# Kernel tuning notes

Hardware: AMD Instinct MI355X
Metric: run time of the kernel (lower is better)

Reference implementation:

```python
import jax, jax.numpy as jnp
import numpy as np

NEG_SLOPE = 0.01  # torch F.leaky_relu default
BN_EPS = 1e-5
N_GRAPHS = 256


def _bn(x, gamma, beta):
    # training-mode BatchNorm1d per head over the node axis; x: [N, H, O]
    mu = x.mean(axis=0)
    var = x.var(axis=0)
    return (x - mu) * jax.lax.rsqrt(var + BN_EPS) * gamma + beta


def _gat_layer(h, src, dst, snorm, fcW, aS, aD, gamma, beta):
    # h: [N, Din]; fcW: [H, Din, O]; aS/aD/gamma/beta: [H, O]
    N = h.shape[0]
    z = jnp.einsum('nd,hdo->nho', h, fcW)                 # [N, H, O]
    el = jnp.einsum('nho,ho->nh', z, aS)                  # attn_fc src half
    er = jnp.einsum('nho,ho->nh', z, aD)                  # attn_fc dst half
    e = jax.nn.leaky_relu(el[src] + er[dst], NEG_SLOPE)   # [E, H]
    emax = jax.ops.segment_max(e, dst, num_segments=N)    # softmax over in-edges
    ee = jnp.exp(e - emax[dst])
    denom = jax.ops.segment_sum(ee, dst, num_segments=N)
    alpha = ee / denom[dst]                               # [E, H]
    msg = alpha[:, :, None] * z[src]                      # [E, H, O]
    agg = jax.ops.segment_sum(msg, dst, num_segments=N)   # [N, H, O]
    agg = agg * snorm[:, None, None]                      # graph_norm
    agg = _bn(agg, gamma, beta)                           # batch_norm
    out = jax.nn.elu(agg).reshape(N, -1)                  # concat heads
    return h + out                                        # residual (Din == H*O)


def setup_inputs() -> dict:
    key = jax.random.key(0)
    ks = jax.random.split(key, 32)
    N, E, G = 50000, 1600000, N_GRAPHS
    DIN, H, O, D, NC = 128, 8, 16, 128, 10
    L_mid = 3  # L-1 multi-head layers

    graph_ids = jnp.sort(jax.random.randint(ks[0], (N,), 0, G))
    counts = jax.ops.segment_sum(jnp.ones((N,), jnp.float32), graph_ids, num_segments=G)
    snorm = (1.0 / jnp.sqrt(jnp.maximum(counts, 1.0)))[graph_ids]  # nodes_num_norm_sqrt
    src = jax.random.randint(ks[1], (E,), 0, N)
    dst = jax.random.randint(ks[2], (E,), 0, N)

    def nrm(k, shape, s=0.1):
        return jax.random.normal(k, shape, jnp.float32) * s

    return {
        'nodes_feat': jax.random.normal(ks[3], (N, DIN), jnp.float32),
        'snorm': snorm,
        'emb_W': nrm(ks[4], (DIN, D)), 'emb_b': jnp.zeros((D,), jnp.float32),
        'fcW': nrm(ks[5], (L_mid, H, D, O)),
        'aS': nrm(ks[6], (L_mid, H, O)), 'aD': nrm(ks[7], (L_mid, H, O)),
        'gamma': jnp.ones((L_mid, H, O), jnp.float32),
        'beta': jnp.zeros((L_mid, H, O), jnp.float32),
        'fcW_last': nrm(ks[8], (1, D, D)),
        'aS_last': nrm(ks[9], (1, D)), 'aD_last': nrm(ks[10], (1, D)),
        'g_last': jnp.ones((1, D), jnp.float32), 'b_last': jnp.zeros((1, D), jnp.float32),
        'w1': nrm(ks[11], (D, D // 2)), 'b1': jnp.zeros((D // 2,), jnp.float32),
        'w2': nrm(ks[12], (D // 2, D // 4)), 'b2': jnp.zeros((D // 4,), jnp.float32),
        'w3': nrm(ks[13], (D // 4, NC)), 'b3': jnp.zeros((NC,), jnp.float32),
        'src': src, 'dst': dst, 'graph_ids': graph_ids,
    }


def reference(nodes_feat, snorm, emb_W, emb_b, fcW, aS, aD, gamma, beta,
              fcW_last, aS_last, aD_last, g_last, b_last,
              w1, b1, w2, b2, w3, b3, src, dst, graph_ids):
    h = nodes_feat @ emb_W + emb_b                        # embedding_h
    for l in range(fcW.shape[0]):                         # L-1 multi-head GAT layers
        h = _gat_layer(h, src, dst, snorm, fcW[l], aS[l], aD[l], gamma[l], beta[l])
    h = _gat_layer(h, src, dst, snorm, fcW_last, aS_last, aD_last, g_last, b_last)
    # mean_nodes readout over variable-size graphs
    counts = jax.ops.segment_sum(jnp.ones_like(snorm), graph_ids, num_segments=N_GRAPHS)
    hg = jax.ops.segment_sum(h, graph_ids, num_segments=N_GRAPHS)
    hg = hg / jnp.maximum(counts, 1.0)[:, None]           # [G, D]
    # MLPReadout: D -> D/2 -> D/4 -> n_classes
    y = jax.nn.relu(hg @ w1 + b1)
    y = jax.nn.relu(y @ w2 + b2)
    return y @ w3 + b3
```

## Files before the change

kernel.cpp:

```cpp
#include <hip/hip_runtime.h>
#include <hip/hip_bf16.h>
#include <hip/hip_fp16.h>

typedef __hip_bfloat16 bf16;
typedef __attribute__((ext_vector_type(8))) short short8;
typedef __attribute__((ext_vector_type(4))) float floatx4;

__device__ __forceinline__ float ldc(const void* p, size_t i, int code) {
    if (code == 1) return __bfloat162float(((const bf16*)p)[i]);
    if (code == 2) return __half2float(((const __half*)p)[i]);
    return ((const float*)p)[i];
}
__device__ __forceinline__ void stc(void* p, size_t i, int code, float v) {
    if (code == 1) ((bf16*)p)[i] = __float2bfloat16(v);
    else if (code == 2) ((__half*)p)[i] = __float2half(v);
    else ((float*)p)[i] = v;
}
__device__ __forceinline__ unsigned int pk2(float a, float b) {
    unsigned int ua = __float_as_uint(a); ua += 0x7fffu + ((ua >> 16) & 1u);
    unsigned int ub = __float_as_uint(b); ub += 0x7fffu + ((ub >> 16) & 1u);
    return (ua >> 16) | (ub & 0xffff0000u);
}

__global__ void k_detect(const unsigned short* __restrict__ g, int* __restrict__ code) {
    unsigned short a = g[0], b = g[1], c = g[2], d = g[3];
    int r;
    if (a == 0x3F80 && b == 0x3F80 && c == 0x3F80 && d == 0x3F80) r = 1;
    else if (a == 0x3C00 && b == 0x3C00 && c == 0x3C00 && d == 0x3C00) r = 2;
    else r = 3;
    *code = r;
}

__global__ void k_zero_i(int* p, int n) { int i = blockIdx.x * 256 + threadIdx.x; if (i < n) p[i] = 0; }
__global__ void k_zero_f(float* p, int n) { int i = blockIdx.x * 256 + threadIdx.x; if (i < n) p[i] = 0.f; }
__global__ void k_sent(void* o, int n, float v, const int* codep) {
    int code = *codep;
    int i = blockIdx.x * 256 + threadIdx.x;
    if (i < n) stc(o, i, code, v);
}

struct CvtArgs { const void* src[17]; int off[18]; };
__global__ void k_cvt_all(float* __restrict__ dst, CvtArgs a,
                          const int* __restrict__ codep, int total) {
    int i = blockIdx.x * 256 + threadIdx.x;
    if (i >= total) return;
    int code = *codep;
    int seg = 0;
    #pragma unroll
    for (int k = 0; k < 16; ++k) seg += (i >= a.off[k + 1]) ? 1 : 0;
    dst[i] = ldc(a.src[seg], i - a.off[seg], code);
}

#define ETILE 8192
__global__ __launch_bounds__(256) void k_bcount(const int* __restrict__ dst,
        int* __restrict__ bcnt, int E, int nbuck) {
    __shared__ int h[200];
    int t = threadIdx.x;
    for (int i = t; i < nbuck; i += 256) h[i] = 0;
    __syncthreads();
    int e0 = blockIdx.x * ETILE;
    int n = min(ETILE, E - e0);
    for (int i = t; i < n; i += 256) atomicAdd(&h[dst[e0 + i] >> 8], 1);
    __syncthreads();
    for (int i = t; i < nbuck; i += 256)
        if (h[i]) atomicAdd(&bcnt[i], h[i]);
}

__global__ void k_scan(const int* __restrict__ cnt, int* __restrict__ off,
                       int* __restrict__ cur, int n) {
    __shared__ int sums[1024];
    int tid = threadIdx.x;
    int C = (n + 1023) >> 10;
    int lo = tid * C, hi = min(lo + C, n);
    int s = 0;
    for (int i = lo; i < hi; ++i) s += cnt[i];
    sums[tid] = s;
    __syncthreads();
    for (int o = 1; o < 1024; o <<= 1) {
        int v = (tid >= o) ? sums[tid - o] : 0;
        __syncthreads();
        sums[tid] += v;
        __syncthreads();
    }
    int run = (tid > 0) ? sums[tid - 1] : 0;
    for (int i = lo; i < hi; ++i) { off[i] = run; cur[i] = run; run += cnt[i]; }
    if (tid == 1023) off[n] = sums[1023];
}

__global__ __launch_bounds__(256) void k_bscat(const int* __restrict__ src,
        const int* __restrict__ dst, int* __restrict__ bcur,
        unsigned int* __restrict__ ebuf, int E, int nbuck) {
    __shared__ unsigned int eord[ETILE];
    __shared__ int cnt[200], lst[200], cur[200], gb[200];
    int t = threadIdx.x;
    int e0 = blockIdx.x * ETILE;
    int n = min(ETILE, E - e0);
    for (int i = t; i < nbuck; i += 256) cnt[i] = 0;
    __syncthreads();
    for (int i = t; i < n; i += 256) atomicAdd(&cnt[dst[e0 + i] >> 8], 1);
    __syncthreads();
    if (t == 0) {
        int run = 0;
        for (int b = 0; b < nbuck; ++b) { int c = cnt[b]; lst[b] = run; cur[b] = run; run += c; }
    }
    __syncthreads();
    for (int b = t; b < nbuck; b += 256)
        gb[b] = cnt[b] ? atomicAdd(&bcur[b], cnt[b]) : 0;
    for (int i = t; i < n; i += 256) {
        int d = dst[e0 + i];
        int pos = atomicAdd(&cur[d >> 8], 1);
        eord[pos] = ((unsigned int)d << 16) | (unsigned int)src[e0 + i];
    }
    __syncthreads();
    for (int i = t; i < n; i += 256) {
        unsigned int pk = eord[i];
        int b = pk >> 24;
        ebuf[gb[b] + (i - lst[b])] = pk;
    }
}

__global__ __launch_bounds__(256) void k_fscatter(const unsigned int* __restrict__ ebuf,
        const int* __restrict__ boff, int* __restrict__ row_off,
        unsigned short* __restrict__ col_src, int N, int E) {
    __shared__ int cnt[256], cur[256];
    int b = blockIdx.x, t = threadIdx.x;
    int lo = boff[b], hi = boff[b + 1];
    int nodelo = b << 8;
    cnt[t] = 0;
    __syncthreads();
    for (int j = lo + t; j < hi; j += 256)
        atomicAdd(&cnt[(int)(ebuf[j] >> 16) - nodelo], 1);
    __syncthreads();
    if (t == 0) {
        int run = lo;
        for (int i = 0; i < 256; ++i) { int c = cnt[i]; cur[i] = run; cnt[i] = run; run += c; }
    }
    __syncthreads();
    int node = nodelo + t;
    if (node < N) row_off[node] = cnt[t];
    if (t == 0 && b == (int)gridDim.x - 1) row_off[N] = E;
    for (int j = lo + t; j < hi; j += 256) {
        unsigned int pk = ebuf[j];
        int pos = atomicAdd(&cur[(int)(pk >> 16) - nodelo], 1);
        col_src[pos] = (unsigned short)(pk & 0xffffu);
    }
}

#define WB_STRIDE 136
#define WB_MAT 19584
__global__ void k_wtrans(const void* __restrict__ fcW, const void* __restrict__ fcW_last,
                         const void* __restrict__ emb_W,
                         const float* __restrict__ aSf, const float* __restrict__ aDf,
                         const float* __restrict__ aSlf, const float* __restrict__ aDlf,
                         unsigned short* __restrict__ Wb, const int* __restrict__ codep) {
    int code = *codep;
    int idx = blockIdx.x * 256 + threadIdx.x;
    if (idx >= 5 * WB_MAT) return;
    int m = idx / WB_MAT, rem = idx % WB_MAT;
    int c = rem / WB_STRIDE, k = rem % WB_STRIDE;
    float v = 0.f;
    if (k < 128) {
        if (m == 0) {
            if (c < 128) v = ldc(emb_W, k * 128 + c, code);
        } else if (m <= 3) {
            int l = m - 1;
            if (c < 128) v = ldc(fcW, l * 16384 + (c >> 4) * 2048 + k * 16 + (c & 15), code);
            else if (c < 136) {
                int hh = c - 128; float s = 0.f;
                for (int o = 0; o < 16; ++o)
                    s += ldc(fcW, l * 16384 + hh * 2048 + k * 16 + o, code) * aSf[l * 128 + hh * 16 + o];
                v = s;
            } else {
                int hh = c - 136; float s = 0.f;
                for (int o = 0; o < 16; ++o)
                    s += ldc(fcW, l * 16384 + hh * 2048 + k * 16 + o, code) * aDf[l * 128 + hh * 16 + o];
                v = s;
            }
        } else {
            if (c < 128) v = ldc(fcW_last, k * 128 + c, code);
            else if (c == 128) { float s = 0.f; for (int o = 0; o < 128; ++o) s += ldc(fcW_last, k * 128 + o, code) * aSlf[o]; v = s; }
            else if (c == 129) { float s = 0.f; for (int o = 0; o < 128; ++o) s += ldc(fcW_last, k * 128 + o, code) * aDlf[o]; v = s; }
        }
    }
    Wb[idx] = (unsigned short)(pk2(v, 0.f) & 0xffffu);
}

__global__ __launch_bounds__(256) void k_gemm(const void* __restrict__ Av, int a_raw,
        const int* __restrict__ codep, const unsigned short* __restrict__ Wbm,
        const float* __restrict__ bias, float* __restrict__ outf,
        unsigned int* __restrict__ zb,
        float* __restrict__ el, float* __restrict__ er, int H, int N) {
    __shared__ unsigned short Wl[WB_MAT];
    int tid = threadIdx.x;
    {
        const uint4* s4 = (const uint4*)Wbm;
        uint4* d4 = (uint4*)Wl;
        for (int i = tid; i < WB_MAT / 8; i += 256) d4[i] = s4[i];
    }
    int wave = tid >> 6, lane = tid & 63;
    int c15 = lane & 15, quad = lane >> 4;
    int rowb = blockIdx.x * 64 + wave * 16;
    int myrow = rowb + c15;
    bool rowok = myrow < N;
    int code = a_raw ? *codep : 3;

    floatx4 acc[9];
    #pragma unroll
    for (int i = 0; i < 9; ++i) acc[i] = (floatx4){0.f, 0.f, 0.f, 0.f};

    __syncthreads();
    #pragma unroll
    for (int ks = 0; ks < 4; ++ks) {
        int k0 = ks * 32 + quad * 8;
        short8 a;
        if (!rowok) {
            a = (short8){0, 0, 0, 0, 0, 0, 0, 0};
        } else if (code == 1) {
            union { uint4 u; short8 s; } cv;
            cv.u = *(const uint4*)((const unsigned short*)Av + (size_t)myrow * 128 + k0);
            a = cv.s;
        } else if (code == 3) {
            const float* ap = (const float*)Av + (size_t)myrow * 128 + k0;
            float4 x = *(const float4*)ap;
            float4 y = *(const float4*)(ap + 4);
            union { uint4 u; short8 s; } cv;
            cv.u = make_uint4(pk2(x.x, x.y), pk2(x.z, x.w), pk2(y.x, y.y), pk2(y.z, y.w));
            a = cv.s;
        } else {
            const __half* ap = (const __half*)Av + (size_t)myrow * 128 + k0;
            union { uint4 u; short8 s; } cv;
            cv.u = make_uint4(pk2(__half2float(ap[0]), __half2float(ap[1])),
                              pk2(__half2float(ap[2]), __half2float(ap[3])),
                              pk2(__half2float(ap[4]), __half2float(ap[5])),
                              pk2(__half2float(ap[6]), __half2float(ap[7])));
            a = cv.s;
        }
        #pragma unroll
        for (int ct = 0; ct < 9; ++ct) {
            union { uint4 u; short8 s; } bv;
            bv.u = *(const uint4*)&Wl[(ct * 16 + c15) * WB_STRIDE + k0];
            acc[ct] = __builtin_amdgcn_mfma_f32_16x16x32_bf16(a, bv.s, acc[ct], 0, 0, 0);
        }
    }

    if (zb == nullptr) {
        #pragma unroll
        for (int ct = 0; ct < 8; ++ct) {
            int c = ct * 16 + c15;
            float bj = bias ? bias[c] : 0.f;
            #pragma unroll
            for (int r = 0; r < 4; ++r) {
                int n = rowb + quad * 4 + r;
                if (n < N) outf[(size_t)n * 128 + c] = acc[ct][r] + bj;
            }
        }
    } else {
        #pragma unroll
        for (int ct = 0; ct < 8; ++ct) {
            #pragma unroll
            for (int r = 0; r < 4; ++r) {
                float v = acc[ct][r];
                float vx = __shfl_xor(v, 1);
                if ((c15 & 1) == 0) {
                    int n = rowb + quad * 4 + r;
                    if (n < N) zb[(size_t)n * 64 + ct * 8 + (c15 >> 1)] = pk2(v, vx);
                }
            }
        }
        #pragma unroll
        for (int r = 0; r < 4; ++r) {
            int n = rowb + quad * 4 + r;
            if (n < N) {
                float v = acc[8][r];
                if (c15 < H) el[n * H + c15] = v;
                else if (c15 < 2 * H) er[n * H + (c15 - H)] = v;
            }
        }
    }
}

__global__ __launch_bounds__(256) void k_agg(const unsigned int* __restrict__ zb,
        const float* __restrict__ el, const float* __restrict__ er,
        const int* __restrict__ row_off, const unsigned short* __restrict__ col_src,
        const float* __restrict__ snormf, float* __restrict__ agg,
        int N, int H) {
    int n = blockIdx.x * 4 + (threadIdx.x >> 6);
    if (n >= N) return;
    int lane = threadIdx.x & 63;
    int half = lane >> 5;
    int sub = lane & 31;
    int hha = (H == 8) ? (sub >> 2) : 0;
    float er_t = er[n * H + hha];
    float er_w = (H == 8) ? er[n * 8 + (lane >> 3)] : er_t;
    int beg = row_off[n], end = row_off[n + 1];
    float l = 0.f, c0 = 0.f, c1 = 0.f, c2 = 0.f, c3 = 0.f;
    int j = beg;
    if (H == 8) {
        for (; j + 8 <= end; j += 8) {
            int sv = col_src[j + (lane & 7)];
            float e = el[sv * 8 + (lane >> 3)] + er_w;
            e = (e > 0.f) ? e : 0.01f * e;
            float w = __expf(fminf(e, 60.f));
            #pragma unroll
            for (int p = 0; p < 4; ++p) {
                int i = 2 * p + half;
                float wi = __shfl(w, (hha << 3) + i);
                int si = col_src[j + i];
                uint2 v = *(const uint2*)(zb + (size_t)si * 64 + sub * 2);
                l += wi;
                c0 = fmaf(wi, __uint_as_float(v.x << 16), c0);
                c1 = fmaf(wi, __uint_as_float(v.x & 0xffff0000u), c1);
                c2 = fmaf(wi, __uint_as_float(v.y << 16), c2);
                c3 = fmaf(wi, __uint_as_float(v.y & 0xffff0000u), c3);
            }
        }
    } else {
        for (; j + 16 <= end; j += 16) {
            int sv = col_src[j + (lane & 15)];
            float e = el[sv] + er_w;
            e = (e > 0.f) ? e : 0.01f * e;
            float w = __expf(fminf(e, 60.f));
            #pragma unroll
            for (int p = 0; p < 8; ++p) {
                int i = 2 * p + half;
                float wi = __shfl(w, i, 16);
                int si = col_src[j + i];
                uint2 v = *(const uint2*)(zb + (size_t)si * 64 + sub * 2);
                l += wi;
                c0 = fmaf(wi, __uint_as_float(v.x << 16), c0);
                c1 = fmaf(wi, __uint_as_float(v.x & 0xffff0000u), c1);
                c2 = fmaf(wi, __uint_as_float(v.y << 16), c2);
                c3 = fmaf(wi, __uint_as_float(v.y & 0xffff0000u), c3);
            }
        }
    }
    for (; j < end; j += 2) {
        int idx = j + half;
        bool act = idx < end;
        int si = col_src[act ? idx : j];
        float e = el[si * H + hha] + er_t;
        e = (e > 0.f) ? e : 0.01f * e;
        float w = act ? __expf(fminf(e, 60.f)) : 0.f;
        uint2 v = *(const uint2*)(zb + (size_t)si * 64 + sub * 2);
        l += w;
        c0 = fmaf(w, __uint_as_float(v.x << 16), c0);
        c1 = fmaf(w, __uint_as_float(v.x & 0xffff0000u), c1);
        c2 = fmaf(w, __uint_as_float(v.y << 16), c2);
        c3 = fmaf(w, __uint_as_float(v.y & 0xffff0000u), c3);
    }
    l  += __shfl_xor(l, 32);
    c0 += __shfl_xor(c0, 32);
    c1 += __shfl_xor(c1, 32);
    c2 += __shfl_xor(c2, 32);
    c3 += __shfl_xor(c3, 32);
    if (half == 0) {
        float sn = snormf[n];
        float inv = (end > beg) ? sn / l : 0.f;
        float4 o = make_float4(c0 * inv, c1 * inv, c2 * inv, c3 * inv);
        *(float4*)&agg[(size_t)n * 128 + 4 * sub] = o;
    }
}

#define BN_BLOCKS 256
__global__ void k_bnstats1(const float* __restrict__ agg, float* __restrict__ pstats, int N) {
    int c = threadIdx.x;
    float s = 0.f, q = 0.f;
    for (int n = blockIdx.x; n < N; n += gridDim.x) {
        float v = agg[(size_t)n * 128 + c];
        s += v; q += v * v;
    }
    pstats[blockIdx.x * 256 + c] = s;
    pstats[blockIdx.x * 256 + 128 + c] = q;
}
__global__ void k_bnstats2(const float* __restrict__ pstats, float* __restrict__ stats, int nb) {
    int c = threadIdx.x;
    float s0 = 0.f, s1 = 0.f, s2 = 0.f, s3 = 0.f;
    int b = 0;
    for (; b + 3 < nb; b += 4) {
        s0 += pstats[b * 256 + c];
        s1 += pstats[(b + 1) * 256 + c];
        s2 += pstats[(b + 2) * 256 + c];
        s3 += pstats[(b + 3) * 256 + c];
    }
    for (; b < nb; ++b) s0 += pstats[b * 256 + c];
    stats[c] = (s0 + s1) + (s2 + s3);
}
__global__ void k_bnapply(const float* __restrict__ agg, const float* __restrict__ stats,
        const float* __restrict__ gamma, const float* __restrict__ beta,
        float* __restrict__ h, int N) {
    int idx = blockIdx.x * 256 + threadIdx.x;
    if (idx >= N * 128) return;
    int c = idx & 127;
    float invN = 1.0f / (float)N;
    float mu = stats[c] * invN;
    float var = fmaxf(stats[128 + c] * invN - mu * mu, 0.f);
    float x = agg[idx];
    float xn = (x - mu) * rsqrtf(var + 1e-5f) * gamma[c] + beta[c];
    float y = (xn > 0.f) ? xn : (__expf(xn) - 1.0f);
    h[idx] += y;
}

__global__ void k_gsum(const float* __restrict__ h, const int* __restrict__ gids,
                       float* __restrict__ hg, float* __restrict__ gcnt, int N) {
    int c = threadIdx.x;
    int base = blockIdx.x * 64;
    int endi = min(base + 64, N);
    int gprev = -1; float acc = 0.f; int cnt = 0;
    for (int n = base; n < endi; ++n) {
        int g = gids[n];
        if (g != gprev) {
            if (gprev >= 0) {
                atomicAdd(&hg[gprev * 128 + c], acc);
                if (c == 0) atomicAdd(&gcnt[gprev], (float)cnt);
            }
            gprev = g; acc = 0.f; cnt = 0;
        }
        acc += h[(size_t)n * 128 + c];
        ++cnt;
    }
    if (gprev >= 0) {
        atomicAdd(&hg[gprev * 128 + c], acc);
        if (c == 0) atomicAdd(&gcnt[gprev], (float)cnt);
    }
}
__global__ void k_mlp(const float* __restrict__ hg, const float* __restrict__ gcnt,
        const float* __restrict__ w1, const float* __restrict__ b1,
        const float* __restrict__ w2, const float* __restrict__ b2,
        const float* __restrict__ w3, const float* __restrict__ b3,
        void* __restrict__ out, const int* __restrict__ codep) {
    __shared__ float xs[128], y1[64], y2[32];
    int g = blockIdx.x, tid = threadIdx.x;
    float inv = 1.0f / fmaxf(gcnt[g], 1.0f);
    xs[tid]      = hg[g * 128 + tid] * inv;
    xs[tid + 64] = hg[g * 128 + 64 + tid] * inv;
    __syncthreads();
    float a = b1[tid];
    for (int k = 0; k < 128; ++k) a = fmaf(xs[k], w1[k * 64 + tid], a);
    y1[tid] = fmaxf(a, 0.f);
    __syncthreads();
    if (tid < 32) {
        float a2 = b2[tid];
        for (int k = 0; k < 64; ++k) a2 = fmaf(y1[k], w2[k * 32 + tid], a2);
        y2[tid] = fmaxf(a2, 0.f);
    }
    __syncthreads();
    if (tid < 10) {
        float a3 = b3[tid];
        for (int k = 0; k < 32; ++k) a3 = fmaf(y2[k], w3[k * 10 + tid], a3);
        stc(out, g * 10 + tid, *codep, a3);
    }
}

extern "C" void kernel_launch(void* const* d_in, const int* in_sizes, int n_in,
                              void* d_out, int out_size, void* d_ws, size_t ws_size,
                              hipStream_t stream) {
    const void* nodes_feat = d_in[0];
    const void* snorm      = d_in[1];
    const void* emb_W      = d_in[2];
    const void* fcW        = d_in[4];
    const void* gamma      = d_in[7];
    const void* fcW_last   = d_in[9];
    const int*  src        = (const int*)d_in[20];
    const int*  dst        = (const int*)d_in[21];
    const int*  gids       = (const int*)d_in[22];

    const int N = 50000, E = 1600000, G = 256;
    const int NBUCK = (N + 255) >> 8;
    const int NTILE = (E + ETILE - 1) / ETILE;
    const int PTOT = 29226 + N;

    char* p = (char*)d_ws;
    auto alloc = [&](size_t bytes) { char* r = p; p += (bytes + 255) & ~(size_t)255; return r; };
    int*   code    = (int*)alloc(256);
    float* h       = (float*)alloc((size_t)N * 128 * 4);
    unsigned int* zb = (unsigned int*)alloc((size_t)N * 64 * 4);
    float* agg     = (float*)alloc((size_t)N * 128 * 4);
    float* el      = (float*)alloc((size_t)N * 8 * 4);
    float* er      = (float*)alloc((size_t)N * 8 * 4);
    int*   bcnt    = (int*)alloc((size_t)NBUCK * 4);
    int*   boff    = (int*)alloc((size_t)(NBUCK + 1) * 4);
    int*   bcur    = (int*)alloc((size_t)NBUCK * 4);
    unsigned int* ebuf = (unsigned int*)alloc((size_t)E * 4);
    int*   row_off = (int*)alloc((size_t)(N + 1) * 4);
    unsigned short* col_src = (unsigned short*)alloc((size_t)E * 2);
    unsigned short* Wb = (unsigned short*)alloc((size_t)5 * WB_MAT * 2);
    float* pstats  = (float*)alloc((size_t)BN_BLOCKS * 256 * 4);
    float* stats   = (float*)alloc(256 * 4);
    float* hg      = (float*)alloc((size_t)G * 128 * 4 + (size_t)G * 4);
    float* gcnt    = hg + (size_t)G * 128;
    float* params  = (float*)alloc((size_t)PTOT * 4);

    const int OFF[18] = {0, 16384, 16512, 16896, 17280, 17664, 18048, 18176,
                         18304, 18432, 18560, 26752, 26816, 28864, 28896, 29216, 29226, PTOT};
    float* emb_bf = params + OFF[1];
    float* aSf    = params + OFF[2];
    float* aDf    = params + OFF[3];
    float* gf     = params + OFF[4];
    float* bf     = params + OFF[5];
    float* aSlf   = params + OFF[6];
    float* aDlf   = params + OFF[7];
    float* glf    = params + OFF[8];
    float* blf    = params + OFF[9];
    float* w1f    = params + OFF[10];
    float* b1f    = params + OFF[11];
    float* w2f    = params + OFF[12];
    float* b2f_   = params + OFF[13];
    float* w3f    = params + OFF[14];
    float* b3f    = params + OFF[15];
    float* snormf = params + OFF[16];

    k_detect<<<1, 1, 0, stream>>>((const unsigned short*)gamma, code);

    bool ok = (n_in == 23) && (out_size == G * 10) &&
              (in_sizes[0] == N * 128) && (in_sizes[1] == N) &&
              (in_sizes[4] == 3 * 8 * 128 * 16) && (in_sizes[7] == 384) &&
              (in_sizes[9] == 16384) &&
              (in_sizes[20] == E) && (in_sizes[21] == E) && (in_sizes[22] == N);
    size_t need = (size_t)(p - (char*)d_ws);
    if (!ok || ws_size < need) {
        k_sent<<<(out_size + 255) / 256, 256, 0, stream>>>(d_out, out_size, ok ? 123.0f : 150.0f, code);
        return;
    }

    CvtArgs ca;
    const int srcidx[17] = {2, 3, 5, 6, 7, 8, 10, 11, 12, 13, 14, 15, 16, 17, 18, 19, 1};
    for (int k = 0; k < 17; ++k) ca.src[k] = d_in[srcidx[k]];
    for (int k = 0; k < 18; ++k) ca.off[k] = OFF[k];
    k_cvt_all<<<(PTOT + 255) / 256, 256, 0, stream>>>(params, ca, code, PTOT);
    k_wtrans<<<(5 * WB_MAT + 255) / 256, 256, 0, stream>>>(
        fcW, fcW_last, emb_W, aSf, aDf, aSlf, aDlf, Wb, code);

    k_zero_i<<<1, 256, 0, stream>>>(bcnt, NBUCK);
    k_bcount<<<NTILE, 256, 0, stream>>>(dst, bcnt, E, NBUCK);
    k_scan<<<1, 1024, 0, stream>>>(bcnt, boff, bcur, NBUCK);
    k_bscat<<<NTILE, 256, 0, stream>>>(src, dst, bcur, ebuf, E, NBUCK);
    k_fscatter<<<NBUCK, 256, 0, stream>>>(ebuf, boff, row_off, col_src, N, E);

    int gblk = (N + 63) / 64;
    k_gemm<<<gblk, 256, 0, stream>>>(nodes_feat, 1, code, Wb, emb_bf, h,
                                     nullptr, nullptr, nullptr, 0, N);

    for (int l = 0; l < 4; ++l) {
        const unsigned short* Wl_ = Wb + (size_t)(l + 1) * WB_MAT;
        const float *gl, *bl; int H;
        if (l < 3) { gl = gf + l * 128; bl = bf + l * 128; H = 8; }
        else       { gl = glf;          bl = blf;          H = 1; }
        k_gemm<<<gblk, 256, 0, stream>>>(h, 0, code, Wl_, nullptr, nullptr,
                                         zb, el, er, H, N);
        k_agg<<<(N + 3) / 4, 256, 0, stream>>>(zb, el, er, row_off, col_src, snormf,
                                               agg, N, H);
        k_bnstats1<<<BN_BLOCKS, 128, 0, stream>>>(agg, pstats, N);
        k_bnstats2<<<1, 256, 0, stream>>>(pstats, stats, BN_BLOCKS);
        k_bnapply<<<(N * 128 + 255) / 256, 256, 0, stream>>>(agg, stats, gl, bl, h, N);
    }

    k_zero_f<<<(G * 129 + 255) / 256, 256, 0, stream>>>(hg, G * 129);
    k_gsum<<<(N + 63) / 64, 128, 0, stream>>>(h, gids, hg, gcnt, N);
    k_mlp<<<G, 64, 0, stream>>>(hg, gcnt, w1f, b1f, w2f, b2f_, w3f, b3f, d_out, code);
}
```

Measured before the change: 921.3 us.

## Software-pipeline neighbor gathers in aggregation and fold BN affine into stats kernel

The edge aggregation loop is restructured so both head configurations process 8 edges per step and prefetch the next block's source indices, attention logits and feature rows while the current block is accumulated. This is meant to hide gather latency on the random-access zb reads. The H=1 path moves from 16-edge to 8-edge batches, and the extra prefetch registers may lower occupancy. BatchNorm is also simplified: the stats kernel now computes a per-channel scale and shift, so the apply kernel does a single fma.

New measurement: 960.1 us. +4.2%, slower.

```diff
diff --git a/kernel.cpp b/kernel.cpp
--- a/kernel.cpp
+++ b/kernel.cpp
@@ -290,48 +290,67 @@
     int half = lane >> 5;
     int sub = lane & 31;
     int hha = (H == 8) ? (sub >> 2) : 0;
+    int wh  = (H == 8) ? (lane >> 3) : 0;
     float er_t = er[n * H + hha];
-    float er_w = (H == 8) ? er[n * 8 + (lane >> 3)] : er_t;
+    float er_w = er[n * H + wh];
     int beg = row_off[n], end = row_off[n + 1];
     float l = 0.f, c0 = 0.f, c1 = 0.f, c2 = 0.f, c3 = 0.f;
+    int nb = (end - beg) >> 3;
     int j = beg;
-    if (H == 8) {
-        for (; j + 8 <= end; j += 8) {
-            int sv = col_src[j + (lane & 7)];
-            float e = el[sv * 8 + (lane >> 3)] + er_w;
-            e = (e > 0.f) ? e : 0.01f * e;
+    if (nb > 0) {
+        int sv = col_src[beg + (lane & 7)];
+        float ew = el[sv * H + wh] + er_w;
+        int s0 = __shfl(sv, half, 8);
+        int s1 = __shfl(sv, 2 + half, 8);
+        int s2 = __shfl(sv, 4 + half, 8);
+        int s3 = __shfl(sv, 6 + half, 8);
+        uint2 v0 = *(const uint2*)(zb + (size_t)s0 * 64 + sub * 2);
+        uint2 v1 = *(const uint2*)(zb + (size_t)s1 * 64 + sub * 2);
+        uint2 v2 = *(const uint2*)(zb + (size_t)s2 * 64 + sub * 2);
+        uint2 v3 = *(const uint2*)(zb + (size_t)s3 * 64 + sub * 2);
+        for (int b = 0; b < nb; ++b) {
+            int jn = j + 8;
+            int sv_n = 0; float ew_n = 0.f;
+            uint2 n0 = make_uint2(0, 0), n1 = n0, n2 = n0, n3 = n0;
+            if (b + 1 < nb) {
+                sv_n = col_src[jn + (lane & 7)];
+                ew_n = el[sv_n * H + wh] + er_w;
+                int t0 = __shfl(sv_n, half, 8);
+                int t1 = __shfl(sv_n, 2 + half, 8);
+                int t2 = __shfl(sv_n, 4 + half, 8);
+                int t3 = __shfl(sv_n, 6 + half, 8);
+                n0 = *(const uint2*)(zb + (size_t)t0 * 64 + sub * 2);
+                n1 = *(const uint2*)(zb + (size_t)t1 * 64 + sub * 2);
+                n2 = *(const uint2*)(zb + (size_t)t2 * 64 + sub * 2);
+                n3 = *(const uint2*)(zb + (size_t)t3 * 64 + sub * 2);
+            }
+            float e = (ew > 0.f) ? ew : 0.01f * ew;
             float w = __expf(fminf(e, 60.f));
-            #pragma unroll
-            for (int p = 0; p < 4; ++p) {
-                int i = 2 * p + half;
-                float wi = __shfl(w, (hha << 3) + i);
-                int si = col_src[j + i];
-                uint2 v = *(const uint2*)(zb + (size_t)si * 64 + sub * 2);
-                l += wi;
-                c0 = fmaf(wi, __uint_as_float(v.x << 16), c0);
-                c1 = fmaf(wi, __uint_as_float(v.x & 0xffff0000u), c1);
-                c2 = fmaf(wi, __uint_as_float(v.y << 16), c2);
-                c3 = fmaf(wi, __uint_as_float(v.y & 0xffff0000u), c3);
-            }
-        }
-    } else {
-        for (; j + 16 <= end; j += 16) {
-            int sv = col_src[j + (lane & 15)];
-            float e = el[sv] + er_w;
-            e = (e > 0.f) ? e : 0.01f * e;
-            float w = __expf(fminf(e, 60.f));
-            #pragma unroll
-            for (int p = 0; p < 8; ++p) {
-                int i = 2 * p + half;
-                float wi = __shfl(w, i, 16);
-                int si = col_src[j + i];
-                uint2 v = *(const uint2*)(zb + (size_t)si * 64 + sub * 2);
-                l += wi;
-                c0 = fmaf(wi, __uint_as_float(v.x << 16), c0);
-                c1 = fmaf(wi, __uint_as_float(v.x & 0xffff0000u), c1);
-                c2 = fmaf(wi, __uint_as_float(v.y << 16), c2);
-                c3 = fmaf(wi, __uint_as_float(v.y & 0xffff0000u), c3);
-            }
+            int wb_ = hha << 3;
+            float w0 = __shfl(w, wb_ + half);
+            float w1 = __shfl(w, wb_ + 2 + half);
+            float w2 = __shfl(w, wb_ + 4 + half);
+            float w3 = __shfl(w, wb_ + 6 + half);
+            l += (w0 + w1) + (w2 + w3);
+            c0 = fmaf(w0, __uint_as_float(v0.x << 16), c0);
+            c1 = fmaf(w0, __uint_as_float(v0.x & 0xffff0000u), c1);
+            c2 = fmaf(w0, __uint_as_float(v0.y << 16), c2);
+            c3 = fmaf(w0, __uint_as_float(v0.y & 0xffff0000u), c3);
+            c0 = fmaf(w1, __uint_as_float(v1.x << 16), c0);
+            c1 = fmaf(w1, __uint_as_float(v1.x & 0xffff0000u), c1);
+            c2 = fmaf(w1, __uint_as_float(v1.y << 16), c2);
+            c3 = fmaf(w1, __uint_as_float(v1.y & 0xffff0000u), c3);
+            c0 = fmaf(w2, __uint_as_float(v2.x << 16), c0);
+            c1 = fmaf(w2, __uint_as_float(v2.x & 0xffff0000u), c1);
+            c2 = fmaf(w2, __uint_as_float(v2.y << 16), c2);
+            c3 = fmaf(w2, __uint_as_float(v2.y & 0xffff0000u), c3);
+            c0 = fmaf(w3, __uint_as_float(v3.x << 16), c0);
+            c1 = fmaf(w3, __uint_as_float(v3.x & 0xffff0000u), c1);
+            c2 = fmaf(w3, __uint_as_float(v3.y << 16), c2);
+            c3 = fmaf(w3, __uint_as_float(v3.y & 0xffff0000u), c3);
+            sv = sv_n; ew = ew_n;
+            v0 = n0; v1 = n1; v2 = n2; v3 = n3;
+            j = jn;
         }
     }
     for (; j < end; j += 2) {
@@ -372,30 +391,32 @@
     pstats[blockIdx.x * 256 + c] = s;
     pstats[blockIdx.x * 256 + 128 + c] = q;
 }
-__global__ void k_bnstats2(const float* __restrict__ pstats, float* __restrict__ stats, int nb) {
+__global__ void k_bnstats2(const float* __restrict__ pstats, float* __restrict__ stats,
+                           const float* __restrict__ gamma, const float* __restrict__ beta,
+                           int nb, float invN) {
     int c = threadIdx.x;
-    float s0 = 0.f, s1 = 0.f, s2 = 0.f, s3 = 0.f;
+    float s0 = 0.f, s1 = 0.f, q0 = 0.f, q1 = 0.f;
     int b = 0;
-    for (; b + 3 < nb; b += 4) {
+    for (; b + 1 < nb; b += 2) {
         s0 += pstats[b * 256 + c];
+        q0 += pstats[b * 256 + 128 + c];
         s1 += pstats[(b + 1) * 256 + c];
-        s2 += pstats[(b + 2) * 256 + c];
-        s3 += pstats[(b + 3) * 256 + c];
-    }
-    for (; b < nb; ++b) s0 += pstats[b * 256 + c];
-    stats[c] = (s0 + s1) + (s2 + s3);
+        q1 += pstats[(b + 1) * 256 + 128 + c];
+    }
+    for (; b < nb; ++b) { s0 += pstats[b * 256 + c]; q0 += pstats[b * 256 + 128 + c]; }
+    float s = s0 + s1, q = q0 + q1;
+    float mu = s * invN;
+    float var = fmaxf(q * invN - mu * mu, 0.f);
+    float A = rsqrtf(var + 1e-5f) * gamma[c];
+    stats[c] = A;
+    stats[128 + c] = fmaf(-mu, A, beta[c]);
 }
 __global__ void k_bnapply(const float* __restrict__ agg, const float* __restrict__ stats,
-        const float* __restrict__ gamma, const float* __restrict__ beta,
         float* __restrict__ h, int N) {
     int idx = blockIdx.x * 256 + threadIdx.x;
     if (idx >= N * 128) return;
     int c = idx & 127;
-    float invN = 1.0f / (float)N;
-    float mu = stats[c] * invN;
-    float var = fmaxf(stats[128 + c] * invN - mu * mu, 0.f);
-    float x = agg[idx];
-    float xn = (x - mu) * rsqrtf(var + 1e-5f) * gamma[c] + beta[c];
+    float xn = fmaf(agg[idx], stats[c], stats[128 + c]);
     float y = (xn > 0.f) ? xn : (__expf(xn) - 1.0f);
     h[idx] += y;
 }
@@ -550,8 +571,8 @@
         k_agg<<<(N + 3) / 4, 256, 0, stream>>>(zb, el, er, row_off, col_src, snormf,
                                                agg, N, H);
         k_bnstats1<<<BN_BLOCKS, 128, 0, stream>>>(agg, pstats, N);
-        k_bnstats2<<<1, 256, 0, stream>>>(pstats, stats, BN_BLOCKS);
-        k_bnapply<<<(N * 128 + 255) / 256, 256, 0, stream>>>(agg, stats, gl, bl, h, N);
+        k_bnstats2<<<1, 128, 0, stream>>>(pstats, stats, gl, bl, BN_BLOCKS, 1.0f / (float)N);
+        k_bnapply<<<(N * 128 + 255) / 256, 256, 0, stream>>>(agg, stats, h, N);
     }
 
     k_zero_f<<<(G * 129 + 255) / 256, 256, 0, stream>>>(hg, G * 129);
```
